# Performance work log

Hardware: AMD Instinct MI355X
Metric: run time of the kernel (lower is better)

The kernel has to match this reference:

```python
import jax, jax.numpy as jnp
import numpy as np

N = 100000   # nodes
E = 1600000  # edges
G = 64       # graphs in batch
H, C = 8, 16 # heads, per-head channels
HID = H * C  # 128
EMB, BBOX, TOK, REL = 256, 32, 151, 51
IN0 = EMB + BBOX  # 288
NEG_SLOPE = 0.2
BN_EPS = 1e-5


def setup_inputs() -> dict:
    key = jax.random.key(0)
    ks = jax.random.split(key, 32)
    f = lambda i, shape: jax.random.normal(ks[i], shape, dtype=jnp.float32) * 0.05
    inp = {}
    inp["tok_id"] = jax.random.randint(ks[0], (N,), 0, TOK)
    inp["bbox"] = jax.random.normal(ks[1], (N, 4), dtype=jnp.float32)
    inp["edge_index"] = jax.random.randint(ks[2], (2, E), 0, N)
    inp["edge_attr"] = jax.random.randint(ks[3], (E,), 0, REL)
    inp["batch"] = jnp.sort(jax.random.randint(ks[4], (N,), 0, G))
    inp["tok_emb"] = f(5, (TOK, EMB))
    inp["bbox_W"] = f(6, (4, BBOX)); inp["bbox_b"] = f(7, (BBOX,))
    inp["rel_emb"] = f(8, (REL, C))
    # layer 0 (in_dim 288 -> 128)
    inp["Wl0"] = f(9, (IN0, HID));  inp["bl0"] = f(10, (HID,))
    inp["Wr0"] = f(11, (IN0, HID)); inp["br0"] = f(12, (HID,))
    inp["We0"] = f(13, (C, HID));   inp["att0"] = f(14, (H, C))
    inp["bias0"] = f(15, (HID,))
    inp["gamma0"] = jnp.ones((HID,), jnp.float32); inp["beta0"] = jnp.zeros((HID,), jnp.float32)
    # layers 1..2 stacked (128 -> 128)
    inp["WlS"] = f(16, (2, HID, HID)); inp["blS"] = f(17, (2, HID))
    inp["WrS"] = f(18, (2, HID, HID)); inp["brS"] = f(19, (2, HID))
    inp["WeS"] = f(20, (2, C, HID));   inp["attS"] = f(21, (2, H, C))
    inp["biasS"] = f(22, (2, HID))
    inp["gammaS"] = jnp.ones((2, HID), jnp.float32); inp["betaS"] = jnp.zeros((2, HID), jnp.float32)
    return inp


def gatv2_layer(x, src, dst, e_emb, Wl, bl, Wr, br, We, att, bias):
    """GATv2Conv: gather -> leaky_relu attention -> segment softmax -> scatter."""
    xl = (x @ Wl + bl).reshape(-1, H, C)   # source transform [N,H,C]
    xr = (x @ Wr + br).reshape(-1, H, C)   # target transform [N,H,C]
    ee = (e_emb @ We).reshape(-1, H, C)    # edge transform  [E,H,C]
    m = jax.nn.leaky_relu(xl[src] + xr[dst] + ee, NEG_SLOPE)  # [E,H,C]
    logits = jnp.einsum('ehc,hc->eh', m, att)                 # [E,H]
    amax = jax.ops.segment_max(logits, dst, num_segments=N)   # [N,H]
    p = jnp.exp(logits - amax[dst])
    denom = jax.ops.segment_sum(p, dst, num_segments=N)       # [N,H]
    alpha = p / jnp.maximum(denom[dst], 1e-16)                # [E,H]
    out = jax.ops.segment_sum(alpha[..., None] * xl[src], dst, num_segments=N)  # [N,H,C]
    return out.reshape(-1, HID) + bias


def batch_norm(x, gamma, beta):
    mu = jnp.mean(x, axis=0)
    var = jnp.var(x, axis=0)
    return gamma * (x - mu) * jax.lax.rsqrt(var + BN_EPS) + beta


def reference(tok_id, bbox, edge_index, edge_attr, batch,
              tok_emb, bbox_W, bbox_b, rel_emb,
              Wl0, bl0, Wr0, br0, We0, att0, bias0, gamma0, beta0,
              WlS, blS, WrS, brS, WeS, attS, biasS, gammaS, betaS):
    src, dst = edge_index[0], edge_index[1]
    x = jnp.concatenate([tok_emb[tok_id], bbox @ bbox_W + bbox_b], axis=-1)  # [N,288]
    e_emb = rel_emb[edge_attr]  # [E,16]
    h = batch_norm(jax.nn.relu(
        gatv2_layer(x, src, dst, e_emb, Wl0, bl0, Wr0, br0, We0, att0, bias0)),
        gamma0, beta0)
    for i in range(2):
        h = h + batch_norm(jax.nn.relu(
            gatv2_layer(h, src, dst, e_emb, WlS[i], blS[i], WrS[i], brS[i], WeS[i], attS[i], biasS[i])),
            gammaS[i], betaS[i])
    # global mean pool over graphs
    sums = jax.ops.segment_sum(h, batch, num_segments=G)
    counts = jax.ops.segment_sum(jnp.ones((h.shape[0],), h.dtype), batch, num_segments=G)
    return sums / jnp.maximum(counts, 1.0)[:, None]  # [G,128]
```

## Files before the change

### kernel.cpp

```cpp
#include <hip/hip_runtime.h>

#define N_NODES 100000
#define N_PAD   100096
#define N_EDGES 1600000
#define NGRAPH  64
#define NHEAD   8
#define NCH     16
#define HID     128
#define IN0     288
#define NREL    51
#define EMB     256
#define NBBOX   32
#define NTOK    151
#define NEG_SLOPE 0.2f
#define EPS_BN  1e-5f
#define AGG_BLOCKS 2048
#define POOL_BLOCKS 1024
#define SENT 0x03F00000u
#define SENT_MIN ((uint)(NREL) << 20)
#define L2E 1.4426950408889634f

typedef unsigned int uint;
typedef unsigned short ushort;

typedef __bf16 bf16_t;
typedef bf16_t bfx8 __attribute__((ext_vector_type(8)));
typedef float  fx4  __attribute__((ext_vector_type(4)));
typedef float  v2f  __attribute__((ext_vector_type(2)));

__device__ __forceinline__ ushort f2bf(float f) {
  uint u = __float_as_uint(f);
  u += 0x7fffu + ((u >> 16) & 1u);
  return (ushort)(u >> 16);
}
__device__ __forceinline__ float bf2f(uint u) { return __uint_as_float(u << 16); }
__device__ __forceinline__ v2f up2(uint u) {
  v2f r;
  r.x = __uint_as_float(u << 16);
  r.y = __uint_as_float(u & 0xffff0000u);
  return r;
}
__device__ __forceinline__ void unpack8(uint4 u, float* f) {
  f[0] = __uint_as_float(u.x << 16); f[1] = __uint_as_float(u.x & 0xffff0000u);
  f[2] = __uint_as_float(u.y << 16); f[3] = __uint_as_float(u.y & 0xffff0000u);
  f[4] = __uint_as_float(u.z << 16); f[5] = __uint_as_float(u.z & 0xffff0000u);
  f[6] = __uint_as_float(u.w << 16); f[7] = __uint_as_float(u.w & 0xffff0000u);
}

__device__ __forceinline__ float w0cat(const float* Wl0, const float* Wr0, int c, int j) {
  return (j < 128) ? Wl0[c * 128 + j] : Wr0[c * 128 + (j - 128)];
}

#define S0 (2 * 256 * HID)
#define S1 (3 * NREL * HID)
#define S2 (3 * 256)
#define S3 (NTOK * 256)
#define S4 (4 * 256)
#define S5 (256)
#define PREP_TOT (S0 + S1 + S2 + S3 + S4 + S5)
__global__ void se_prep(const float* __restrict__ Wl0, const float* __restrict__ Wr0,
                        const float* __restrict__ WlS, const float* __restrict__ WrS,
                        const float* __restrict__ rel_emb, const float* __restrict__ We0,
                        const float* __restrict__ WeS,
                        const float* __restrict__ bl0, const float* __restrict__ br0,
                        const float* __restrict__ blS, const float* __restrict__ brS,
                        const float* __restrict__ tok_emb, const float* __restrict__ bbox_W,
                        const float* __restrict__ bbox_b,
                        ushort* __restrict__ WST, float* __restrict__ eetab,
                        float* __restrict__ biascat,
                        float* __restrict__ T, float* __restrict__ F, float* __restrict__ cvec) {
  int i = blockIdx.x * 256 + threadIdx.x;
  if (i < S0) {
    int li = i >> 15;
    int rem = i & 32767;
    int j = rem >> 7, k = rem & 127;
    float v = (j < 128) ? WlS[(li * 128 + k) * 128 + j] : WrS[(li * 128 + k) * 128 + (j - 128)];
    WST[(li * 256 + j) * 128 + k] = f2bf(v);
    return;
  }
  i -= S0;
  if (i < S1) {
    int li = i / (NREL * HID);
    int rem = i - li * (NREL * HID);
    int r = rem >> 7, j = rem & 127;
    const float* We = (li == 0) ? We0 : (WeS + (li - 1) * NCH * HID);
    float s = 0.f;
#pragma unroll
    for (int c = 0; c < NCH; c++) s += rel_emb[r * NCH + c] * We[c * HID + j];
    eetab[li * (NREL * HID) + rem] = s;
    return;
  }
  i -= S1;
  if (i < S2) {
    int li = i >> 8, j = i & 255;
    const float* bl = (li == 0) ? bl0 : (blS + (li - 1) * HID);
    const float* br = (li == 0) ? br0 : (brS + (li - 1) * HID);
    biascat[i] = (j < 128) ? bl[j] : br[j - 128];
    return;
  }
  i -= S2;
  if (i < S3) {
    int t = i >> 8, j = i & 255;
    float s = 0.f;
    for (int c = 0; c < EMB; c++) s += tok_emb[t * EMB + c] * w0cat(Wl0, Wr0, c, j);
    T[i] = s;
    return;
  }
  i -= S3;
  if (i < S4) {
    int r = i >> 8, j = i & 255;
    float s = 0.f;
#pragma unroll
    for (int b = 0; b < NBBOX; b++) s += bbox_W[r * NBBOX + b] * w0cat(Wl0, Wr0, EMB + b, j);
    F[i] = s;
    return;
  }
  i -= S4;
  if (i < S5) {
    int j = i;
    float s = (j < 128) ? bl0[j] : br0[j - 128];
#pragma unroll
    for (int b = 0; b < NBBOX; b++) s += bbox_b[b] * w0cat(Wl0, Wr0, EMB + b, j);
    cvec[j] = s;
  }
}

__global__ void se_xform0(const int* __restrict__ tok_id, const float* __restrict__ bbox,
                          const float* __restrict__ T, const float* __restrict__ F,
                          const float* __restrict__ cvec, ushort* __restrict__ xlxr) {
  int idx = blockIdx.x * 256 + threadIdx.x;
  if (idx >= N_NODES * 32) return;
  const int n = idx >> 5, k = idx & 31;
  const int j0 = k * 8;
  const int t = tok_id[n];
  const float4 bb = *(const float4*)(bbox + (size_t)n * 4);
  float o[8];
#pragma unroll
  for (int h = 0; h < 2; h++) {
    const float4 tv = *(const float4*)(T + t * 256 + j0 + 4 * h);
    const float4 cv = *(const float4*)(cvec + j0 + 4 * h);
    const float4 f0 = *(const float4*)(F + 0 * 256 + j0 + 4 * h);
    const float4 f1 = *(const float4*)(F + 1 * 256 + j0 + 4 * h);
    const float4 f2 = *(const float4*)(F + 2 * 256 + j0 + 4 * h);
    const float4 f3 = *(const float4*)(F + 3 * 256 + j0 + 4 * h);
    o[4 * h + 0] = tv.x + cv.x + bb.x * f0.x + bb.y * f1.x + bb.z * f2.x + bb.w * f3.x;
    o[4 * h + 1] = tv.y + cv.y + bb.x * f0.y + bb.y * f1.y + bb.z * f2.y + bb.w * f3.y;
    o[4 * h + 2] = tv.z + cv.z + bb.x * f0.z + bb.y * f1.z + bb.z * f2.z + bb.w * f3.z;
    o[4 * h + 3] = tv.w + cv.w + bb.x * f0.w + bb.y * f1.w + bb.z * f2.w + bb.w * f3.w;
  }
  uint4 p;
  p.x = ((uint)f2bf(o[1]) << 16) | f2bf(o[0]);
  p.y = ((uint)f2bf(o[3]) << 16) | f2bf(o[2]);
  p.z = ((uint)f2bf(o[5]) << 16) | f2bf(o[4]);
  p.w = ((uint)f2bf(o[7]) << 16) | f2bf(o[6]);
  ((uint4*)xlxr)[idx] = p;
}

__global__ void se_hist(const int* __restrict__ ei, int* __restrict__ deg) {
  int e = blockIdx.x * 256 + threadIdx.x;
  if (e < N_EDGES) atomicAdd(&deg[ei[N_EDGES + e]], 1);
}
__global__ __launch_bounds__(1024) void se_scanA(const int* __restrict__ deg,
                                                 int* __restrict__ offs, int* __restrict__ bsum) {
  __shared__ int s[1024];
  const int tid = threadIdx.x;
  const int i = blockIdx.x * 1024 + tid;
  int v = (i < N_NODES) ? ((deg[i] + 3) & ~3) : 0;
  s[tid] = v;
  __syncthreads();
  for (int d = 1; d < 1024; d <<= 1) {
    int t = (tid >= d) ? s[tid - d] : 0;
    __syncthreads();
    s[tid] += t;
    __syncthreads();
  }
  if (i < N_NODES) offs[i] = s[tid] - v;
  if (tid == 1023) bsum[blockIdx.x] = s[1023];
}
__global__ __launch_bounds__(128) void se_scanB(int* __restrict__ bsum, int nb) {
  __shared__ int s[128];
  const int t = threadIdx.x;
  int v = (t < nb) ? bsum[t] : 0;
  s[t] = v;
  __syncthreads();
  for (int d = 1; d < 128; d <<= 1) {
    int u = (t >= d) ? s[t - d] : 0;
    __syncthreads();
    s[t] += u;
    __syncthreads();
  }
  if (t < nb) bsum[t] = s[t] - v;
}
__global__ __launch_bounds__(1024) void se_scanC(int* __restrict__ offs, const int* __restrict__ bsum) {
  int i = blockIdx.x * 1024 + threadIdx.x;
  if (i < N_NODES) offs[i] += bsum[blockIdx.x];
}
__global__ void se_padfill(const int* __restrict__ deg, const int* __restrict__ offs,
                           uint* __restrict__ csrp, int2* __restrict__ rowinfo) {
  int n = blockIdx.x * 256 + threadIdx.x;
  if (n >= N_NODES) return;
  const int d = deg[n];
  const int o = offs[n];
  rowinfo[n] = make_int2(o, (d + 3) >> 2);
  const int s = o + d;
  const int c = ((d + 3) & ~3) - d;
  for (int j = 0; j < c; j++) csrp[s + j] = SENT;
  if (n == N_NODES - 1) {
    const int e = o + ((d + 3) & ~3);
    for (int j = 0; j < 64; j++) csrp[e + j] = SENT;
  }
}
__global__ void se_scatter(const int* __restrict__ ei, const int* __restrict__ eattr,
                           const int* __restrict__ offs, int* __restrict__ cur,
                           uint* __restrict__ csrp) {
  int e = blockIdx.x * 256 + threadIdx.x;
  if (e < N_EDGES) {
    int d = ei[N_EDGES + e];
    int p = offs[d] + atomicAdd(&cur[d], 1);
    csrp[p] = (uint)ei[e] | ((uint)eattr[e] << 20);
  }
}

template <int K>
__global__ __launch_bounds__(256) void se_gemm(const ushort* __restrict__ A,
                                               const ushort* __restrict__ BT,
                                               const float* __restrict__ bias,
                                               ushort* __restrict__ C) {
  __shared__ __align__(16) ushort As[128 * 32];
  __shared__ __align__(16) ushort Bs[128 * 32];
  const int tid = threadIdx.x;
  const int w = tid >> 6, l = tid & 63;
  const int wr = w >> 1, wc = w & 1;
  const int m0 = blockIdx.x * 128, n0 = blockIdx.y * 128;
  fx4 acc[4][4];
#pragma unroll
  for (int i = 0; i < 4; i++)
#pragma unroll
    for (int j = 0; j < 4; j++) acc[i][j] = fx4{0.f, 0.f, 0.f, 0.f};

  for (int k0 = 0; k0 < K; k0 += 32) {
#pragma unroll
    for (int ch = 0; ch < 2; ch++) {
      const int t = tid + ch * 256;
      const int r = t >> 2, c = (t & 3) << 3;
      const ushort* ga = A + (size_t)(m0 + r) * K + (k0 + c);
      ushort* la = As + (size_t)(ch * 256 + w * 64) * 8;
      __builtin_amdgcn_global_load_lds((const __attribute__((address_space(1))) void*)ga,
                                       (__attribute__((address_space(3))) void*)la, 16, 0, 0);
      const ushort* gb = BT + (size_t)(n0 + r) * K + (k0 + c);
      ushort* lb = Bs + (size_t)(ch * 256 + w * 64) * 8;
      __builtin_amdgcn_global_load_lds((const __attribute__((address_space(1))) void*)gb,
                                       (__attribute__((address_space(3))) void*)lb, 16, 0, 0);
    }
    __syncthreads();
    bfx8 af[4], bfr[4];
#pragma unroll
    for (int i = 0; i < 4; i++) {
      af[i]  = *(const bfx8*)(As + ((wr * 64 + i * 16 + (l & 15)) * 32 + ((l >> 4) * 8)));
      bfr[i] = *(const bfx8*)(Bs + ((wc * 64 + i * 16 + (l & 15)) * 32 + ((l >> 4) * 8)));
    }
#pragma unroll
    for (int i = 0; i < 4; i++)
#pragma unroll
      for (int j = 0; j < 4; j++)
        acc[i][j] = __builtin_amdgcn_mfma_f32_16x16x32_bf16(af[i], bfr[j], acc[i][j], 0, 0, 0);
    __syncthreads();
  }
#pragma unroll
  for (int i = 0; i < 4; i++) {
    const int rbase = m0 + wr * 64 + i * 16 + ((l >> 4) << 2);
#pragma unroll
    for (int j = 0; j < 4; j++) {
      const int col = n0 + wc * 64 + j * 16 + (l & 15);
      const float bz = bias[col];
#pragma unroll
      for (int r2 = 0; r2 < 4; r2++) {
        const int row = rbase + r2;
        if (row < N_NODES) C[(size_t)row * 256 + col] = f2bf(acc[i][j][r2] + bz);
      }
    }
  }
}

__global__ __launch_bounds__(256) void se_agg(const uint4* __restrict__ xlxr4,
                                              const uint* __restrict__ csrp,
                                              const int2* __restrict__ rowinfo,
                                              const float* __restrict__ eetab,
                                              const float* __restrict__ att,
                                              const float* __restrict__ bias,
                                              float* __restrict__ y, float* __restrict__ partial) {
  __shared__ float ee[64 * HID];
  __shared__ float bstat[256];
  const int tid = threadIdx.x, w = tid >> 6, l = tid & 63;
  const int g = l >> 4, k = l & 15;
  for (int i = tid; i < 64 * HID; i += 256) {
    const int r = i >> 7;
    ee[i] = (r < NREL) ? eetab[i] : 0.f;
  }
  bstat[tid] = 0.f;
  __syncthreads();
  v2f av[4];
  {
    const float* ap = att + (k >> 1) * NCH + (k & 1) * 8;
#pragma unroll
    for (int q = 0; q < 4; q++) av[q] = v2f{ap[2 * q] * L2E, ap[2 * q + 1] * L2E};
  }
  v2f sv[4], qv[4];
#pragma unroll
  for (int q = 0; q < 4; q++) { sv[q] = v2f{0.f, 0.f}; qv[q] = v2f{0.f, 0.f}; }
  const v2f zero = v2f{0.f, 0.f};

  const int stride = gridDim.x * 4;
  for (int n = blockIdx.x * 4 + w; n < N_NODES; n += stride) {
    const int2 ri = rowinfo[n];
    const uint* rowp = csrp + ri.x + g;
    const int nit = ri.y;
    v2f xrv[4];
    {
      const uint4 xru = xlxr4[(uint)n * 32u + 16u + (uint)k];
      xrv[0] = up2(xru.x); xrv[1] = up2(xru.y); xrv[2] = up2(xru.z); xrv[3] = up2(xru.w);
    }
    float den = 0.f;
    v2f acc[4];
#pragma unroll
    for (int q = 0; q < 4; q++) acc[q] = zero;

    uint eA = SENT, eB = SENT;
    uint4 xlv = uint4{0u, 0u, 0u, 0u};
    if (nit > 0) {
      eA = rowp[0];
      xlv = xlxr4[(eA & 0xFFFFFu) * 32u + (uint)k];
      if (nit > 1) eB = rowp[4];
    }
#pragma unroll 2
    for (int i = 0; i < nit; ++i) {
      const uint ec = eA;
      const uint4 xc = xlv;
      eA = eB;
      if (i + 1 < nit) xlv = xlxr4[(eA & 0xFFFFFu) * 32u + (uint)k];
      if (i + 2 < nit) eB = rowp[4 * (i + 2)];
      const float* eerow = ee + (ec >> 20) * HID + k * 8;
      const float4 e0v = *(const float4*)(eerow);
      const float4 e1v = *(const float4*)(eerow + 4);
      const v2f eef[4] = {v2f{e0v.x, e0v.y}, v2f{e0v.z, e0v.w},
                          v2f{e1v.x, e1v.y}, v2f{e1v.z, e1v.w}};
      v2f sd = zero;
      v2f xls[4];
      {
        const uint xcu[4] = {xc.x, xc.y, xc.z, xc.w};
#pragma unroll
        for (int q = 0; q < 4; q++) {
          const v2f xl = up2(xcu[q]);
          const v2f m = xl + xrv[q] + eef[q];
          const v2f lk = __builtin_elementwise_max(m, NEG_SLOPE * m);
          sd += lk * av[q];
          xls[q] = xl;
        }
      }
      float s = sd.x + sd.y;
      s += __shfl_xor(s, 1);
      s = (ec >= SENT_MIN) ? -1e30f : s;
      const float p = exp2f(s);
      den += p;
      const v2f pp = v2f{p, p};
#pragma unroll
      for (int q = 0; q < 4; q++) acc[q] += pp * xls[q];
    }
    den += __shfl_xor(den, 16);
    den += __shfl_xor(den, 32);
#pragma unroll
    for (int q = 0; q < 4; q++) {
      acc[q].x += __shfl_xor(acc[q].x, 16); acc[q].x += __shfl_xor(acc[q].x, 32);
      acc[q].y += __shfl_xor(acc[q].y, 16); acc[q].y += __shfl_xor(acc[q].y, 32);
    }
    if (g == 0) {
      const float r = 1.f / fmaxf(den, 1e-16f);
      const v2f rr = v2f{r, r};
      const float4 b0 = ((const float4*)bias)[k * 2];
      const float4 b1 = ((const float4*)bias)[k * 2 + 1];
      const v2f bv[4] = {v2f{b0.x, b0.y}, v2f{b0.z, b0.w}, v2f{b1.x, b1.y}, v2f{b1.z, b1.w}};
      v2f ov[4];
#pragma unroll
      for (int q = 0; q < 4; q++) {
        ov[q] = __builtin_elementwise_max(acc[q] * rr + bv[q], zero);
        sv[q] += ov[q];
        qv[q] += ov[q] * ov[q];
      }
      float4* yp = (float4*)y + (size_t)n * 32 + (size_t)k * 2;
      yp[0] = make_float4(ov[0].x, ov[0].y, ov[1].x, ov[1].y);
      yp[1] = make_float4(ov[2].x, ov[2].y, ov[3].x, ov[3].y);
    }
  }
  if (l < 16) {
#pragma unroll
    for (int q = 0; q < 4; q++) {
      unsafeAtomicAdd(&bstat[k * 8 + 2 * q], sv[q].x);
      unsafeAtomicAdd(&bstat[k * 8 + 2 * q + 1], sv[q].y);
      unsafeAtomicAdd(&bstat[128 + k * 8 + 2 * q], qv[q].x);
      unsafeAtomicAdd(&bstat[128 + k * 8 + 2 * q + 1], qv[q].y);
    }
  }
  __syncthreads();
  partial[(size_t)tid * AGG_BLOCKS + blockIdx.x] = bstat[tid];
}

__global__ __launch_bounds__(256) void se_stats(const float* __restrict__ partial, float* __restrict__ musig) {
  __shared__ float red[256];
  const int ch = blockIdx.x, tid = threadIdx.x;
  float s = 0.f;
  for (int i = tid; i < AGG_BLOCKS; i += 256) s += partial[ch * AGG_BLOCKS + i];
  red[tid] = s; __syncthreads();
  for (int o = 128; o > 0; o >>= 1) { if (tid < o) red[tid] += red[tid + o]; __syncthreads(); }
  const float sum = red[0]; __syncthreads();
  float q = 0.f;
  for (int i = tid; i < AGG_BLOCKS; i += 256) q += partial[(128 + ch) * AGG_BLOCKS + i];
  red[tid] = q; __syncthreads();
  for (int o = 128; o > 0; o >>= 1) { if (tid < o) red[tid] += red[tid + o]; __syncthreads(); }
  if (tid == 0) {
    const float mean = sum / (float)N_NODES;
    const float var = red[0] / (float)N_NODES - mean * mean;
    musig[ch] = mean;
    musig[128 + ch] = rsqrtf(var + EPS_BN);
  }
}

__global__ void se_bn(const float* __restrict__ y, const float* __restrict__ musig,
                      const float* __restrict__ gamma, const float* __restrict__ beta,
                      ushort* __restrict__ h_bf, int residual) {
  int idx = blockIdx.x * 256 + threadIdx.x;
  if (idx >= N_NODES * 16) return;
  const int k = idx & 15;
  const float4 y0 = ((const float4*)y)[(size_t)idx * 2];
  const float4 y1 = ((const float4*)y)[(size_t)idx * 2 + 1];
  const float4 mu0 = ((const float4*)musig)[k * 2],         mu1 = ((const float4*)musig)[k * 2 + 1];
  const float4 rs0 = ((const float4*)(musig + 128))[k * 2], rs1 = ((const float4*)(musig + 128))[k * 2 + 1];
  const float4 g0  = ((const float4*)gamma)[k * 2],         g1  = ((const float4*)gamma)[k * 2 + 1];
  const float4 b0  = ((const float4*)beta)[k * 2],          b1  = ((const float4*)beta)[k * 2 + 1];
  float v[8];
  v[0] = g0.x * (y0.x - mu0.x) * rs0.x + b0.x;
  v[1] = g0.y * (y0.y - mu0.y) * rs0.y + b0.y;
  v[2] = g0.z * (y0.z - mu0.z) * rs0.z + b0.z;
  v[3] = g0.w * (y0.w - mu0.w) * rs0.w + b0.w;
  v[4] = g1.x * (y1.x - mu1.x) * rs1.x + b1.x;
  v[5] = g1.y * (y1.y - mu1.y) * rs1.y + b1.y;
  v[6] = g1.z * (y1.z - mu1.z) * rs1.z + b1.z;
  v[7] = g1.w * (y1.w - mu1.w) * rs1.w + b1.w;
  if (residual) {
    const uint4 ho = ((const uint4*)h_bf)[idx];
    float fr[8];
    unpack8(ho, fr);
#pragma unroll
    for (int j = 0; j < 8; j++) v[j] += fr[j];
  }
  uint4 p4;
  p4.x = ((uint)f2bf(v[1]) << 16) | f2bf(v[0]);
  p4.y = ((uint)f2bf(v[3]) << 16) | f2bf(v[2]);
  p4.z = ((uint)f2bf(v[5]) << 16) | f2bf(v[4]);
  p4.w = ((uint)f2bf(v[7]) << 16) | f2bf(v[6]);
  ((uint4*)h_bf)[idx] = p4;
}

__global__ __launch_bounds__(256) void se_pool(const ushort* __restrict__ h_bf,
                                               const int* __restrict__ batch,
                                               float* __restrict__ pool) {
  const int tid = threadIdx.x, w = tid >> 6, l = tid & 63;
  const int wid = blockIdx.x * 4 + w;
  const int nw = gridDim.x * 4;
  const int chunk = (N_NODES + nw - 1) / nw;
  const int start = wid * chunk;
  const int end = min(N_NODES, start + chunk);
  float a0 = 0.f, a1 = 0.f;
  int cg = -1, cnt = 0;
  for (int n = start; n < end; ++n) {
    const int gg = batch[n];
    if (gg != cg) {
      if (cg >= 0) {
        unsafeAtomicAdd(&pool[cg * HID + 2 * l], a0);
        unsafeAtomicAdd(&pool[cg * HID + 2 * l + 1], a1);
        if (l == 0) unsafeAtomicAdd(&pool[NGRAPH * HID + cg], (float)cnt);
      }
      a0 = 0.f; a1 = 0.f; cnt = 0; cg = gg;
    }
    const uint u = ((const uint*)h_bf)[(size_t)n * 64 + l];
    a0 += bf2f(u & 0xffffu);
    a1 += __uint_as_float(u & 0xffff0000u);
    cnt++;
  }
  if (cg >= 0) {
    unsafeAtomicAdd(&pool[cg * HID + 2 * l], a0);
    unsafeAtomicAdd(&pool[cg * HID + 2 * l + 1], a1);
    if (l == 0) unsafeAtomicAdd(&pool[NGRAPH * HID + cg], (float)cnt);
  }
}
__global__ void se_poolfin(const float* __restrict__ pool, float* __restrict__ out) {
  int idx = blockIdx.x * 256 + threadIdx.x;
  if (idx < NGRAPH * HID) {
    int g = idx >> 7;
    out[idx] = pool[idx] / fmaxf(pool[NGRAPH * HID + g], 1.f);
  }
}

extern "C" void kernel_launch(void* const* d_in, const int* in_sizes, int n_in,
                              void* d_out, int out_size, void* d_ws, size_t ws_size,
                              hipStream_t stream) {
  (void)in_sizes; (void)n_in; (void)out_size; (void)ws_size;
  const int*   tok_id  = (const int*)d_in[0];
  const float* bbox    = (const float*)d_in[1];
  const int*   ei      = (const int*)d_in[2];
  const int*   eattr   = (const int*)d_in[3];
  const int*   batch   = (const int*)d_in[4];
  const float* tok_emb = (const float*)d_in[5];
  const float* bbox_W  = (const float*)d_in[6];
  const float* bbox_b  = (const float*)d_in[7];
  const float* rel_emb = (const float*)d_in[8];
  const float* Wl0  = (const float*)d_in[9];
  const float* bl0  = (const float*)d_in[10];
  const float* Wr0  = (const float*)d_in[11];
  const float* br0  = (const float*)d_in[12];
  const float* We0  = (const float*)d_in[13];
  const float* att0 = (const float*)d_in[14];
  const float* bias0  = (const float*)d_in[15];
  const float* gamma0 = (const float*)d_in[16];
  const float* beta0  = (const float*)d_in[17];
  const float* WlS  = (const float*)d_in[18];
  const float* blS  = (const float*)d_in[19];
  const float* WrS  = (const float*)d_in[20];
  const float* brS  = (const float*)d_in[21];
  const float* WeS  = (const float*)d_in[22];
  const float* attS = (const float*)d_in[23];
  const float* biasS  = (const float*)d_in[24];
  const float* gammaS = (const float*)d_in[25];
  const float* betaS  = (const float*)d_in[26];
  float* out = (float*)d_out;

  char* ws = (char*)d_ws;
  size_t off = 0;
  auto alloc = [&](size_t bytes) -> char* {
    char* p = ws + off;
    off = (off + bytes + 255) & ~(size_t)255;
    return p;
  };
  ushort* xlxr = (ushort*)alloc((size_t)N_PAD * 256 * 2);
  float*  y    = (float*)alloc((size_t)N_NODES * HID * 4);
  ushort* h_bf = (ushort*)alloc((size_t)N_PAD * HID * 2);
  ushort* WST  = (ushort*)alloc((size_t)2 * 256 * HID * 2);
  float*  eetab   = (float*)alloc((size_t)3 * NREL * HID * 4);
  float*  biascat = (float*)alloc((size_t)3 * 256 * 4);
  float*  T    = (float*)alloc((size_t)NTOK * 256 * 4);
  float*  F    = (float*)alloc((size_t)4 * 256 * 4);
  float*  cvec = (float*)alloc((size_t)256 * 4);
  char*  z0   = ws + off;
  int*   deg  = (int*)alloc((size_t)N_NODES * 4);
  int*   cur  = (int*)alloc((size_t)N_NODES * 4);
  float* pool = (float*)alloc((size_t)(NGRAPH * HID + NGRAPH) * 4);
  size_t zlen = (size_t)((ws + off) - z0);
  int* offs = (int*)alloc((size_t)(N_NODES + 1) * 4);
  int* bsum = (int*)alloc(128 * 4);
  int2* rowinfo = (int2*)alloc((size_t)N_NODES * 8);
  uint* csrp = (uint*)alloc((size_t)(N_EDGES + 3 * N_NODES + 256) * 4);
  float* partial = (float*)alloc((size_t)256 * AGG_BLOCKS * 4);
  float* musig   = (float*)alloc(256 * 4);

  hipMemsetAsync(z0, 0, zlen, stream);

  se_prep<<<(PREP_TOT + 255) / 256, 256, 0, stream>>>(
      Wl0, Wr0, WlS, WrS, rel_emb, We0, WeS, bl0, br0, blS, brS,
      tok_emb, bbox_W, bbox_b, WST, eetab, biascat, T, F, cvec);
  se_hist<<<(N_EDGES + 255) / 256, 256, 0, stream>>>(ei, deg);
  se_scanA<<<98, 1024, 0, stream>>>(deg, offs, bsum);
  se_scanB<<<1, 128, 0, stream>>>(bsum, 98);
  se_scanC<<<98, 1024, 0, stream>>>(offs, bsum);
  se_padfill<<<(N_NODES + 255) / 256, 256, 0, stream>>>(deg, offs, csrp, rowinfo);
  se_scatter<<<(N_EDGES + 255) / 256, 256, 0, stream>>>(ei, eattr, offs, cur, csrp);

  se_xform0<<<(N_NODES * 32 + 255) / 256, 256, 0, stream>>>(tok_id, bbox, T, F, cvec, xlxr);
  se_agg<<<AGG_BLOCKS, 256, 0, stream>>>((const uint4*)xlxr, csrp, rowinfo,
                                         eetab, att0, bias0, y, partial);
  se_stats<<<128, 256, 0, stream>>>(partial, musig);
  se_bn<<<(N_NODES * 16 + 255) / 256, 256, 0, stream>>>(y, musig, gamma0, beta0, h_bf, 0);

  for (int li = 0; li < 2; ++li) {
    se_gemm<HID><<<dim3(N_PAD / 128, 2), 256, 0, stream>>>(h_bf, WST + (size_t)li * 256 * HID,
                                                           biascat + (li + 1) * 256, xlxr);
    se_agg<<<AGG_BLOCKS, 256, 0, stream>>>((const uint4*)xlxr, csrp, rowinfo,
                                           eetab + (size_t)(li + 1) * NREL * HID,
                                           attS + (size_t)li * NHEAD * NCH,
                                           biasS + (size_t)li * HID, y, partial);
    se_stats<<<128, 256, 0, stream>>>(partial, musig);
    se_bn<<<(N_NODES * 16 + 255) / 256, 256, 0, stream>>>(y, musig, gammaS + (size_t)li * HID,
                                                          betaS + (size_t)li * HID, h_bf, 1);
  }

  se_pool<<<POOL_BLOCKS, 256, 0, stream>>>(h_bf, batch, pool);
  se_poolfin<<<32, 256, 0, stream>>>(pool, out);
}
```

Baseline: 814.7 us.

## Remap aggregation to one head per lane with 8 edge groups and bf16 edge table

The aggregation kernel now gives each lane a full head (16 channels) instead of half a head, and processes 8 edges in parallel per wavefront instead of 4. This drops the per-edge cross-lane shuffle for the attention logit, and CSR rows are padded to multiples of 8 to match. The edge-embedding table in shared memory is stored as bf16, halving LDS reads, and the scan-add and pad-fill kernels are fused into one launch. In exchange, registers per lane roughly double and padding adds more wasted sentinel edges for low-degree nodes.

```diff
diff --git a/kernel.cpp b/kernel.cpp
--- a/kernel.cpp
+++ b/kernel.cpp
@@ -165,7 +165,7 @@
   __shared__ int s[1024];
   const int tid = threadIdx.x;
   const int i = blockIdx.x * 1024 + tid;
-  int v = (i < N_NODES) ? ((deg[i] + 3) & ~3) : 0;
+  int v = (i < N_NODES) ? ((deg[i] + 7) & ~7) : 0;
   s[tid] = v;
   __syncthreads();
   for (int d = 1; d < 1024; d <<= 1) {
@@ -191,22 +191,22 @@
   }
   if (t < nb) bsum[t] = s[t] - v;
 }
-__global__ __launch_bounds__(1024) void se_scanC(int* __restrict__ offs, const int* __restrict__ bsum) {
+__global__ __launch_bounds__(1024) void se_scanC_pad(int* __restrict__ offs,
+                                                     const int* __restrict__ bsum,
+                                                     const int* __restrict__ deg,
+                                                     uint* __restrict__ csrp,
+                                                     int2* __restrict__ rowinfo) {
   int i = blockIdx.x * 1024 + threadIdx.x;
-  if (i < N_NODES) offs[i] += bsum[blockIdx.x];
-}
-__global__ void se_padfill(const int* __restrict__ deg, const int* __restrict__ offs,
-                           uint* __restrict__ csrp, int2* __restrict__ rowinfo) {
-  int n = blockIdx.x * 256 + threadIdx.x;
-  if (n >= N_NODES) return;
-  const int d = deg[n];
-  const int o = offs[n];
-  rowinfo[n] = make_int2(o, (d + 3) >> 2);
+  if (i >= N_NODES) return;
+  const int o = offs[i] + bsum[blockIdx.x];
+  offs[i] = o;
+  const int d = deg[i];
+  rowinfo[i] = make_int2(o, (d + 7) >> 3);
   const int s = o + d;
-  const int c = ((d + 3) & ~3) - d;
+  const int c = ((d + 7) & ~7) - d;
   for (int j = 0; j < c; j++) csrp[s + j] = SENT;
-  if (n == N_NODES - 1) {
-    const int e = o + ((d + 3) & ~3);
+  if (i == N_NODES - 1) {
+    const int e = o + ((d + 7) & ~7);
     for (int j = 0; j < 64; j++) csrp[e + j] = SENT;
   }
 }
@@ -289,25 +289,25 @@
                                               const float* __restrict__ att,
                                               const float* __restrict__ bias,
                                               float* __restrict__ y, float* __restrict__ partial) {
-  __shared__ float ee[64 * HID];
+  __shared__ ushort ee[64 * HID];
   __shared__ float bstat[256];
   const int tid = threadIdx.x, w = tid >> 6, l = tid & 63;
-  const int g = l >> 4, k = l & 15;
+  const int g = l >> 3, j = l & 7;
   for (int i = tid; i < 64 * HID; i += 256) {
     const int r = i >> 7;
-    ee[i] = (r < NREL) ? eetab[i] : 0.f;
+    ee[i] = (r < NREL) ? f2bf(eetab[i]) : (ushort)0;
   }
   bstat[tid] = 0.f;
   __syncthreads();
-  v2f av[4];
+  v2f av[8];
   {
-    const float* ap = att + (k >> 1) * NCH + (k & 1) * 8;
-#pragma unroll
-    for (int q = 0; q < 4; q++) av[q] = v2f{ap[2 * q] * L2E, ap[2 * q + 1] * L2E};
-  }
-  v2f sv[4], qv[4];
-#pragma unroll
-  for (int q = 0; q < 4; q++) { sv[q] = v2f{0.f, 0.f}; qv[q] = v2f{0.f, 0.f}; }
+    const float* ap = att + j * NCH;
+#pragma unroll
+    for (int q = 0; q < 8; q++) av[q] = v2f{ap[2 * q] * L2E, ap[2 * q + 1] * L2E};
+  }
+  v2f sv[8], qv[8];
+#pragma unroll
+  for (int q = 0; q < 8; q++) { sv[q] = v2f{0.f, 0.f}; qv[q] = v2f{0.f, 0.f}; }
   const v2f zero = v2f{0.f, 0.f};
 
   const int stride = gridDim.x * 4;
@@ -315,89 +315,94 @@
     const int2 ri = rowinfo[n];
     const uint* rowp = csrp + ri.x + g;
     const int nit = ri.y;
-    v2f xrv[4];
+    v2f xrv[8];
     {
-      const uint4 xru = xlxr4[(uint)n * 32u + 16u + (uint)k];
-      xrv[0] = up2(xru.x); xrv[1] = up2(xru.y); xrv[2] = up2(xru.z); xrv[3] = up2(xru.w);
+      const uint b = (uint)n * 32u + 16u + (uint)(j * 2);
+      const uint4 x0 = xlxr4[b], x1 = xlxr4[b + 1u];
+      xrv[0] = up2(x0.x); xrv[1] = up2(x0.y); xrv[2] = up2(x0.z); xrv[3] = up2(x0.w);
+      xrv[4] = up2(x1.x); xrv[5] = up2(x1.y); xrv[6] = up2(x1.z); xrv[7] = up2(x1.w);
     }
     float den = 0.f;
-    v2f acc[4];
-#pragma unroll
-    for (int q = 0; q < 4; q++) acc[q] = zero;
+    v2f acc[8];
+#pragma unroll
+    for (int q = 0; q < 8; q++) acc[q] = zero;
 
     uint eA = SENT, eB = SENT;
-    uint4 xlv = uint4{0u, 0u, 0u, 0u};
+    uint4 xa0 = uint4{0u, 0u, 0u, 0u}, xa1 = uint4{0u, 0u, 0u, 0u};
     if (nit > 0) {
       eA = rowp[0];
-      xlv = xlxr4[(eA & 0xFFFFFu) * 32u + (uint)k];
-      if (nit > 1) eB = rowp[4];
-    }
-#pragma unroll 2
+      const uint s0 = (eA & 0xFFFFFu) * 32u + (uint)(j * 2);
+      xa0 = xlxr4[s0]; xa1 = xlxr4[s0 + 1u];
+      if (nit > 1) eB = rowp[8];
+    }
     for (int i = 0; i < nit; ++i) {
       const uint ec = eA;
-      const uint4 xc = xlv;
+      const uint4 xc0 = xa0, xc1 = xa1;
       eA = eB;
-      if (i + 1 < nit) xlv = xlxr4[(eA & 0xFFFFFu) * 32u + (uint)k];
-      if (i + 2 < nit) eB = rowp[4 * (i + 2)];
-      const float* eerow = ee + (ec >> 20) * HID + k * 8;
-      const float4 e0v = *(const float4*)(eerow);
-      const float4 e1v = *(const float4*)(eerow + 4);
-      const v2f eef[4] = {v2f{e0v.x, e0v.y}, v2f{e0v.z, e0v.w},
-                          v2f{e1v.x, e1v.y}, v2f{e1v.z, e1v.w}};
+      if (i + 1 < nit) {
+        const uint s1 = (eA & 0xFFFFFu) * 32u + (uint)(j * 2);
+        xa0 = xlxr4[s1]; xa1 = xlxr4[s1 + 1u];
+      }
+      if (i + 2 < nit) eB = rowp[8 * (i + 2)];
+      const ushort* eerow = ee + (ec >> 20) * HID + j * 16;
+      const uint4 eu0 = *(const uint4*)(eerow);
+      const uint4 eu1 = *(const uint4*)(eerow + 8);
       v2f sd = zero;
-      v2f xls[4];
+      v2f xls[8];
       {
-        const uint xcu[4] = {xc.x, xc.y, xc.z, xc.w};
-#pragma unroll
-        for (int q = 0; q < 4; q++) {
+        const uint xcu[8] = {xc0.x, xc0.y, xc0.z, xc0.w, xc1.x, xc1.y, xc1.z, xc1.w};
+        const uint eu[8]  = {eu0.x, eu0.y, eu0.z, eu0.w, eu1.x, eu1.y, eu1.z, eu1.w};
+#pragma unroll
+        for (int q = 0; q < 8; q++) {
           const v2f xl = up2(xcu[q]);
-          const v2f m = xl + xrv[q] + eef[q];
+          const v2f m = xl + xrv[q] + up2(eu[q]);
           const v2f lk = __builtin_elementwise_max(m, NEG_SLOPE * m);
           sd += lk * av[q];
           xls[q] = xl;
         }
       }
       float s = sd.x + sd.y;
-      s += __shfl_xor(s, 1);
       s = (ec >= SENT_MIN) ? -1e30f : s;
       const float p = exp2f(s);
       den += p;
       const v2f pp = v2f{p, p};
 #pragma unroll
-      for (int q = 0; q < 4; q++) acc[q] += pp * xls[q];
-    }
-    den += __shfl_xor(den, 16);
-    den += __shfl_xor(den, 32);
-#pragma unroll
-    for (int q = 0; q < 4; q++) {
-      acc[q].x += __shfl_xor(acc[q].x, 16); acc[q].x += __shfl_xor(acc[q].x, 32);
-      acc[q].y += __shfl_xor(acc[q].y, 16); acc[q].y += __shfl_xor(acc[q].y, 32);
+      for (int q = 0; q < 8; q++) acc[q] += pp * xls[q];
+    }
+#pragma unroll
+    for (int lvl = 8; lvl <= 32; lvl <<= 1) {
+      den += __shfl_xor(den, lvl);
+#pragma unroll
+      for (int q = 0; q < 8; q++) {
+        acc[q].x += __shfl_xor(acc[q].x, lvl);
+        acc[q].y += __shfl_xor(acc[q].y, lvl);
+      }
     }
     if (g == 0) {
       const float r = 1.f / fmaxf(den, 1e-16f);
       const v2f rr = v2f{r, r};
-      const float4 b0 = ((const float4*)bias)[k * 2];
-      const float4 b1 = ((const float4*)bias)[k * 2 + 1];
-      const v2f bv[4] = {v2f{b0.x, b0.y}, v2f{b0.z, b0.w}, v2f{b1.x, b1.y}, v2f{b1.z, b1.w}};
-      v2f ov[4];
-#pragma unroll
-      for (int q = 0; q < 4; q++) {
-        ov[q] = __builtin_elementwise_max(acc[q] * rr + bv[q], zero);
+      const float* bp = bias + j * 16;
+      v2f ov[8];
+#pragma unroll
+      for (int q = 0; q < 8; q++) {
+        ov[q] = __builtin_elementwise_max(acc[q] * rr + v2f{bp[2 * q], bp[2 * q + 1]}, zero);
         sv[q] += ov[q];
         qv[q] += ov[q] * ov[q];
       }
-      float4* yp = (float4*)y + (size_t)n * 32 + (size_t)k * 2;
+      float4* yp = (float4*)(y + (size_t)n * HID + j * 16);
       yp[0] = make_float4(ov[0].x, ov[0].y, ov[1].x, ov[1].y);
       yp[1] = make_float4(ov[2].x, ov[2].y, ov[3].x, ov[3].y);
-    }
-  }
-  if (l < 16) {
-#pragma unroll
-    for (int q = 0; q < 4; q++) {
-      unsafeAtomicAdd(&bstat[k * 8 + 2 * q], sv[q].x);
-      unsafeAtomicAdd(&bstat[k * 8 + 2 * q + 1], sv[q].y);
-      unsafeAtomicAdd(&bstat[128 + k * 8 + 2 * q], qv[q].x);
-      unsafeAtomicAdd(&bstat[128 + k * 8 + 2 * q + 1], qv[q].y);
+      yp[2] = make_float4(ov[4].x, ov[4].y, ov[5].x, ov[5].y);
+      yp[3] = make_float4(ov[6].x, ov[6].y, ov[7].x, ov[7].y);
+    }
+  }
+  if (l < 8) {
+#pragma unroll
+    for (int q = 0; q < 8; q++) {
+      unsafeAtomicAdd(&bstat[j * 16 + 2 * q], sv[q].x);
+      unsafeAtomicAdd(&bstat[j * 16 + 2 * q + 1], sv[q].y);
+      unsafeAtomicAdd(&bstat[128 + j * 16 + 2 * q], qv[q].x);
+      unsafeAtomicAdd(&bstat[128 + j * 16 + 2 * q + 1], qv[q].y);
     }
   }
   __syncthreads();
@@ -557,7 +562,7 @@
   int* offs = (int*)alloc((size_t)(N_NODES + 1) * 4);
   int* bsum = (int*)alloc(128 * 4);
   int2* rowinfo = (int2*)alloc((size_t)N_NODES * 8);
-  uint* csrp = (uint*)alloc((size_t)(N_EDGES + 3 * N_NODES + 256) * 4);
+  uint* csrp = (uint*)alloc((size_t)(N_EDGES + 7 * N_NODES + 256) * 4);
   float* partial = (float*)alloc((size_t)256 * AGG_BLOCKS * 4);
   float* musig   = (float*)alloc(256 * 4);
 
@@ -569,8 +574,7 @@
   se_hist<<<(N_EDGES + 255) / 256, 256, 0, stream>>>(ei, deg);
   se_scanA<<<98, 1024, 0, stream>>>(deg, offs, bsum);
   se_scanB<<<1, 128, 0, stream>>>(bsum, 98);
-  se_scanC<<<98, 1024, 0, stream>>>(offs, bsum);
-  se_padfill<<<(N_NODES + 255) / 256, 256, 0, stream>>>(deg, offs, csrp, rowinfo);
+  se_scanC_pad<<<98, 1024, 0, stream>>>(offs, bsum, deg, csrp, rowinfo);
   se_scatter<<<(N_EDGES + 255) / 256, 256, 0, stream>>>(ei, eattr, offs, cur, csrp);
 
   se_xform0<<<(N_NODES * 32 + 255) / 256, 256, 0, stream>>>(tok_id, bbox, T, F, cvec, xlxr);
```

Result: slower. 904.2 us (+11.0%).

## Prefetch next node's first edge across node loop, bf16 edge table, fuse scan+padfill

Applied to the files above, without the earlier changes.

The aggregation kernel now software-pipelines across nodes: while reducing and writing the current node it already loads the next node's rowinfo, first CSR entry and first xl gather, hiding the head-of-row latency chain. The shared-memory edge-embedding table is stored as bf16 instead of fp32, halving LDS footprint and read width at a small precision cost. The scan fix-up and padding-fill kernels are merged into one launch. Dropping the unroll pragma and holding more live registers could affect occupancy.

```diff
diff --git a/kernel.cpp b/kernel.cpp
--- a/kernel.cpp
+++ b/kernel.cpp
@@ -191,21 +191,21 @@
   }
   if (t < nb) bsum[t] = s[t] - v;
 }
-__global__ __launch_bounds__(1024) void se_scanC(int* __restrict__ offs, const int* __restrict__ bsum) {
+__global__ __launch_bounds__(1024) void se_scanC_pad(int* __restrict__ offs,
+                                                     const int* __restrict__ bsum,
+                                                     const int* __restrict__ deg,
+                                                     uint* __restrict__ csrp,
+                                                     int2* __restrict__ rowinfo) {
   int i = blockIdx.x * 1024 + threadIdx.x;
-  if (i < N_NODES) offs[i] += bsum[blockIdx.x];
-}
-__global__ void se_padfill(const int* __restrict__ deg, const int* __restrict__ offs,
-                           uint* __restrict__ csrp, int2* __restrict__ rowinfo) {
-  int n = blockIdx.x * 256 + threadIdx.x;
-  if (n >= N_NODES) return;
-  const int d = deg[n];
-  const int o = offs[n];
-  rowinfo[n] = make_int2(o, (d + 3) >> 2);
+  if (i >= N_NODES) return;
+  const int o = offs[i] + bsum[blockIdx.x];
+  offs[i] = o;
+  const int d = deg[i];
+  rowinfo[i] = make_int2(o, (d + 3) >> 2);
   const int s = o + d;
   const int c = ((d + 3) & ~3) - d;
   for (int j = 0; j < c; j++) csrp[s + j] = SENT;
-  if (n == N_NODES - 1) {
+  if (i == N_NODES - 1) {
     const int e = o + ((d + 3) & ~3);
     for (int j = 0; j < 64; j++) csrp[e + j] = SENT;
   }
@@ -289,13 +289,13 @@
                                               const float* __restrict__ att,
                                               const float* __restrict__ bias,
                                               float* __restrict__ y, float* __restrict__ partial) {
-  __shared__ float ee[64 * HID];
+  __shared__ ushort ee[64 * HID];
   __shared__ float bstat[256];
   const int tid = threadIdx.x, w = tid >> 6, l = tid & 63;
   const int g = l >> 4, k = l & 15;
   for (int i = tid; i < 64 * HID; i += 256) {
     const int r = i >> 7;
-    ee[i] = (r < NREL) ? eetab[i] : 0.f;
+    ee[i] = (r < NREL) ? f2bf(eetab[i]) : (ushort)0;
   }
   bstat[tid] = 0.f;
   __syncthreads();
@@ -311,47 +311,47 @@
   const v2f zero = v2f{0.f, 0.f};
 
   const int stride = gridDim.x * 4;
-  for (int n = blockIdx.x * 4 + w; n < N_NODES; n += stride) {
-    const int2 ri = rowinfo[n];
+  int n = blockIdx.x * 4 + w;
+  int2 ri = make_int2(0, 0);
+  uint eA = SENT;
+  uint4 xlv = uint4{0u, 0u, 0u, 0u};
+  if (n < N_NODES) {
+    ri = rowinfo[n];
+    eA = csrp[ri.x + g];
+    xlv = xlxr4[(eA & 0xFFFFFu) * 32u + (uint)k];
+  }
+  while (n < N_NODES) {
+    const int n2 = n + stride;
+    int2 ri2 = make_int2(0, 0);
+    if (n2 < N_NODES) ri2 = rowinfo[n2];
+    const uint4 xru = xlxr4[(uint)n * 32u + 16u + (uint)k];
     const uint* rowp = csrp + ri.x + g;
     const int nit = ri.y;
+    uint eB = SENT;
+    if (nit > 1) eB = rowp[4];
     v2f xrv[4];
-    {
-      const uint4 xru = xlxr4[(uint)n * 32u + 16u + (uint)k];
-      xrv[0] = up2(xru.x); xrv[1] = up2(xru.y); xrv[2] = up2(xru.z); xrv[3] = up2(xru.w);
-    }
+    xrv[0] = up2(xru.x); xrv[1] = up2(xru.y); xrv[2] = up2(xru.z); xrv[3] = up2(xru.w);
     float den = 0.f;
     v2f acc[4];
 #pragma unroll
     for (int q = 0; q < 4; q++) acc[q] = zero;
 
-    uint eA = SENT, eB = SENT;
-    uint4 xlv = uint4{0u, 0u, 0u, 0u};
-    if (nit > 0) {
-      eA = rowp[0];
-      xlv = xlxr4[(eA & 0xFFFFFu) * 32u + (uint)k];
-      if (nit > 1) eB = rowp[4];
-    }
-#pragma unroll 2
     for (int i = 0; i < nit; ++i) {
       const uint ec = eA;
       const uint4 xc = xlv;
       eA = eB;
       if (i + 1 < nit) xlv = xlxr4[(eA & 0xFFFFFu) * 32u + (uint)k];
       if (i + 2 < nit) eB = rowp[4 * (i + 2)];
-      const float* eerow = ee + (ec >> 20) * HID + k * 8;
-      const float4 e0v = *(const float4*)(eerow);
-      const float4 e1v = *(const float4*)(eerow + 4);
-      const v2f eef[4] = {v2f{e0v.x, e0v.y}, v2f{e0v.z, e0v.w},
-                          v2f{e1v.x, e1v.y}, v2f{e1v.z, e1v.w}};
+      const uint4 eeu = *(const uint4*)(ee + (ec >> 20) * HID + k * 8);
       v2f sd = zero;
       v2f xls[4];
       {
         const uint xcu[4] = {xc.x, xc.y, xc.z, xc.w};
+        const uint eu[4] = {eeu.x, eeu.y, eeu.z, eeu.w};
 #pragma unroll
         for (int q = 0; q < 4; q++) {
           const v2f xl = up2(xcu[q]);
-          const v2f m = xl + xrv[q] + eef[q];
+          const v2f m = xl + xrv[q] + up2(eu[q]);
           const v2f lk = __builtin_elementwise_max(m, NEG_SLOPE * m);
           sd += lk * av[q];
           xls[q] = xl;
@@ -366,6 +366,8 @@
 #pragma unroll
       for (int q = 0; q < 4; q++) acc[q] += pp * xls[q];
     }
+    uint eA2 = SENT;
+    if (n2 < N_NODES) eA2 = csrp[ri2.x + g];
     den += __shfl_xor(den, 16);
     den += __shfl_xor(den, 32);
 #pragma unroll
@@ -373,6 +375,8 @@
       acc[q].x += __shfl_xor(acc[q].x, 16); acc[q].x += __shfl_xor(acc[q].x, 32);
       acc[q].y += __shfl_xor(acc[q].y, 16); acc[q].y += __shfl_xor(acc[q].y, 32);
     }
+    uint4 xlv2 = uint4{0u, 0u, 0u, 0u};
+    if (n2 < N_NODES) xlv2 = xlxr4[(eA2 & 0xFFFFFu) * 32u + (uint)k];
     if (g == 0) {
       const float r = 1.f / fmaxf(den, 1e-16f);
       const v2f rr = v2f{r, r};
@@ -390,6 +394,7 @@
       yp[0] = make_float4(ov[0].x, ov[0].y, ov[1].x, ov[1].y);
       yp[1] = make_float4(ov[2].x, ov[2].y, ov[3].x, ov[3].y);
     }
+    n = n2; ri = ri2; eA = eA2; xlv = xlv2;
   }
   if (l < 16) {
 #pragma unroll
@@ -569,8 +574,7 @@
   se_hist<<<(N_EDGES + 255) / 256, 256, 0, stream>>>(ei, deg);
   se_scanA<<<98, 1024, 0, stream>>>(deg, offs, bsum);
   se_scanB<<<1, 128, 0, stream>>>(bsum, 98);
-  se_scanC<<<98, 1024, 0, stream>>>(offs, bsum);
-  se_padfill<<<(N_NODES + 255) / 256, 256, 0, stream>>>(deg, offs, csrp, rowinfo);
+  se_scanC_pad<<<98, 1024, 0, stream>>>(offs, bsum, deg, csrp, rowinfo);
   se_scatter<<<(N_EDGES + 255) / 256, 256, 0, stream>>>(ei, eattr, offs, cur, csrp);
 
   se_xform0<<<(N_NODES * 32 + 255) / 256, 256, 0, stream>>>(tok_id, bbox, T, F, cvec, xlxr);
```

Result: no change. 810.7 us (-0.5%).
